# Kernel optimization log

Hardware: AMD Instinct MI355X
Metric: run time of the kernel (lower is better)

Reference implementation:

```python
import jax, jax.numpy as jnp
import numpy as np

DK_SCALE = 1.0 / np.sqrt(64.0).astype(np.float32)  # 1/sqrt(d_k)
TEMPERATURE = 1.0  # __init__ overrides temperature to 1
MASK_FILL = -1000000000.0


def setup_inputs() -> dict:
    key = jax.random.key(0)
    kq, kk, kv, km = jax.random.split(key, 4)
    B, H, S, D = 4, 16, 2048, 64
    q = jax.random.normal(kq, (B, H, S, D), dtype=jnp.float32)
    k = jax.random.normal(kk, (B, H, S, D), dtype=jnp.float32)
    v = jax.random.normal(kv, (B, H, S, D), dtype=jnp.float32)
    mask = jax.random.randint(km, (B, 1, S, S), 0, 2, dtype=jnp.int32)
    return {"q": q, "k": k, "v": v, "mask": mask}


def reference(q, k, v, mask):
    # attn = (q * scale) @ k^T  -> [B, H, S, S]
    scale = jnp.asarray(DK_SCALE / TEMPERATURE, dtype=q.dtype)
    attn = jnp.einsum("bhqd,bhkd->bhqk", q * scale, k)
    attn = jnp.where(mask == 0, jnp.asarray(MASK_FILL, dtype=attn.dtype), attn)
    attn = jax.nn.softmax(attn, axis=-1)
    out = jnp.einsum("bhqk,bhkd->bhqd", attn, v)
    return (out, attn)
```

## Files before the change

### kernel.cpp

```cpp
#include <hip/hip_runtime.h>
#include <hip/hip_bf16.h>


#define NB 4
#define NH 16
#define S_ 2048
#define D_ 64
#define QT 16
#define NW 8
#define NT 512
#define KSEG (S_ / NW)
#define SCALE 0.125f
#define MASKFILL -1000000000.0f

typedef float f32x4 __attribute__((ext_vector_type(4)));
typedef int   i32x4 __attribute__((ext_vector_type(4)));
typedef short bf16x8 __attribute__((ext_vector_type(8)));

__device__ __forceinline__ short f2bf(float x) {
  union { __hip_bfloat16 h; short s; } u;
  u.h = __float2bfloat16(x);
  return u.s;
}

__global__ __launch_bounds__(NT, 2)
void sdpa_fused(const float* __restrict__ q, const float* __restrict__ k,
                const float* __restrict__ v, const int* __restrict__ mask,
                float* __restrict__ out, float* __restrict__ attn)
{
  __shared__ float sc[QT * S_];

  const int qt   = blockIdx.x;
  const int bh   = blockIdx.y;
  const int b    = bh >> 4;
  const int tid  = threadIdx.x;
  const int wid  = tid >> 6;
  const int lane = tid & 63;
  const int l15  = lane & 15;
  const int l4   = lane >> 4;

  const float* __restrict__ qh = q + (size_t)bh * S_ * D_;
  const float* __restrict__ kh = k + (size_t)bh * S_ * D_;
  const float* __restrict__ vh = v + (size_t)bh * S_ * D_;
  const int*   __restrict__ mb = mask + (size_t)b * S_ * S_;
  const int q0 = qt * QT;

  bf16x8 aq[2];
  {
    const float* qrow = qh + (size_t)(q0 + l15) * D_ + l4 * 8;
    #pragma unroll
    for (int h = 0; h < 2; ++h) {
      f32x4 x0 = *(const f32x4*)(qrow + h * 32);
      f32x4 x1 = *(const f32x4*)(qrow + h * 32 + 4);
      bf16x8 a;
      #pragma unroll
      for (int j = 0; j < 4; ++j) {
        a[j]     = f2bf(x0[j] * SCALE);
        a[j + 4] = f2bf(x1[j] * SCALE);
      }
      aq[h] = a;
    }
  }

  const int kbase = wid * KSEG;
  #pragma unroll 2
  for (int g = 0; g < KSEG / 16; ++g) {
    const int kc = kbase + g * 16;
    const float* krow = kh + (size_t)(kc + l15) * D_ + l4 * 8;
    f32x4 acc = {0.f, 0.f, 0.f, 0.f};
    #pragma unroll
    for (int h = 0; h < 2; ++h) {
      f32x4 x0 = *(const f32x4*)(krow + h * 32);
      f32x4 x1 = *(const f32x4*)(krow + h * 32 + 4);
      bf16x8 bk;
      #pragma unroll
      for (int j = 0; j < 4; ++j) { bk[j] = f2bf(x0[j]); bk[j + 4] = f2bf(x1[j]); }
      acc = __builtin_amdgcn_mfma_f32_16x16x32_bf16(aq[h], bk, acc, 0, 0, 0);
    }
    #pragma unroll
    for (int r = 0; r < 4; ++r) {
      const int row = l4 * 4 + r;
      const int col = kc + l15;
      sc[row * S_ + ((((col >> 2) ^ row) << 2) | (col & 3))] = acc[r];
    }
  }
  __syncthreads();

  #pragma unroll
  for (int rr = 0; rr < 2; ++rr) {
    const int row = wid * 2 + rr;
    float* srow = sc + row * S_;
    const int* mrow = mb + (size_t)(q0 + row) * S_;

    f32x4 m4 = {-3.0e38f, -3.0e38f, -3.0e38f, -3.0e38f};
    for (int i = 0; i < 8; ++i) {
      const int clin = i * 64 + lane;
      const int c = (clin ^ row) << 2;
      f32x4 vv = *(f32x4*)(srow + c);
      i32x4 mm = *(const i32x4*)(mrow + clin * 4);
      #pragma unroll
      for (int j = 0; j < 4; ++j) {
        vv[j] = mm[j] ? vv[j] : MASKFILL;
        m4[j] = fmaxf(m4[j], vv[j]);
      }
      *(f32x4*)(srow + c) = vv;
    }
    float mx = fmaxf(fmaxf(m4[0], m4[1]), fmaxf(m4[2], m4[3]));
    #pragma unroll
    for (int off = 32; off >= 1; off >>= 1) mx = fmaxf(mx, __shfl_xor(mx, off));

    f32x4 s4 = {0.f, 0.f, 0.f, 0.f};
    for (int i = 0; i < 8; ++i) {
      const int c = ((i * 64 + lane) ^ row) << 2;
      f32x4 vv = *(f32x4*)(srow + c);
      f32x4 e;
      #pragma unroll
      for (int j = 0; j < 4; ++j) { e[j] = __expf(vv[j] - mx); s4[j] += e[j]; }
      *(f32x4*)(srow + c) = e;
    }
    float sm = s4[0] + s4[1] + s4[2] + s4[3];
    #pragma unroll
    for (int off = 32; off >= 1; off >>= 1) sm += __shfl_xor(sm, off);
    const float rinv = 1.0f / sm;

    float* arow = attn + ((size_t)bh * S_ + q0 + row) * S_;
    for (int i = 0; i < 8; ++i) {
      const int clin = i * 64 + lane;
      const int c = (clin ^ row) << 2;
      f32x4 vv = *(f32x4*)(srow + c);
      vv *= rinv;
      *(f32x4*)(srow + c) = vv;
      *(f32x4*)(arow + clin * 4) = vv;
    }
  }
  __syncthreads();

  f32x4 oacc[4] = {{0,0,0,0},{0,0,0,0},{0,0,0,0},{0,0,0,0}};
  #pragma unroll 2
  for (int ks = 0; ks < KSEG; ks += 32) {
    const int k0 = kbase + ks + l4 * 8;
    const float* srow = sc + l15 * S_;
    const int cc = k0 >> 2;
    f32x4 p0 = *(const f32x4*)(srow + ((cc ^ l15) << 2));
    f32x4 p1 = *(const f32x4*)(srow + (((cc + 1) ^ l15) << 2));
    bf16x8 ap;
    #pragma unroll
    for (int j = 0; j < 4; ++j) { ap[j] = f2bf(p0[j]); ap[j + 4] = f2bf(p1[j]); }
    #pragma unroll
    for (int g = 0; g < 4; ++g) {
      bf16x8 bv;
      #pragma unroll
      for (int j = 0; j < 8; ++j)
        bv[j] = f2bf(vh[(size_t)(k0 + j) * D_ + g * 16 + l15]);
      oacc[g] = __builtin_amdgcn_mfma_f32_16x16x32_bf16(ap, bv, oacc[g], 0, 0, 0);
    }
  }
  __syncthreads();

  float* part = sc;
  #pragma unroll
  for (int g = 0; g < 4; ++g) {
    #pragma unroll
    for (int r = 0; r < 4; ++r)
      part[(wid * QT + l4 * 4 + r) * D_ + g * 16 + l15] = oacc[g][r];
  }
  __syncthreads();

  float* orow = out + ((size_t)bh * S_ + q0) * D_;
  for (int o = tid; o < QT * D_; o += NT) {
    float s = 0.f;
    #pragma unroll
    for (int w = 0; w < NW; ++w) s += part[w * (QT * D_) + o];
    orow[o] = s;
  }
}

extern "C" void kernel_launch(void* const* d_in, const int* in_sizes, int n_in,
                              void* d_out, int out_size, void* d_ws, size_t ws_size,
                              hipStream_t stream) {
  const float* q    = (const float*)d_in[0];
  const float* k    = (const float*)d_in[1];
  const float* v    = (const float*)d_in[2];
  const int*   mask = (const int*)d_in[3];
  float* out  = (float*)d_out;
  float* attn = out + (size_t)NB * NH * S_ * D_;
  dim3 grid(S_ / QT, NB * NH);
  sdpa_fused<<<grid, dim3(NT), 0, stream>>>(q, k, v, mask, out, attn);
}
```

Measured before the change: 1.991 ms.

## Keep attention scores in registers and cut shared memory for higher occupancy

The 128KB shared score buffer is replaced by per-wave register accumulators (16 fragments of QK^T). Row max and sum are combined across waves through small shared buffers. Probabilities are packed as bf16 in registers, written to attn with nontemporal stores, and staged through a small per-wave LDS tile for the PV MFMA. Other changes: a 1D grid with block swizzling for L2 locality, launch bounds raised to 4 blocks per CU, and masks read directly in MFMA fragment layout. The cost is higher register pressure and normalized attn values that are rounded from bf16-packed exponentials, which lowers precision.

```diff
diff --git a/kernel.cpp b/kernel.cpp
--- a/kernel.cpp
+++ b/kernel.cpp
@@ -9,12 +9,12 @@
 #define QT 16
 #define NW 8
 #define NT 512
-#define KSEG (S_ / NW)
+#define KSEG 256
+#define NF 16
 #define SCALE 0.125f
 #define MASKFILL -1000000000.0f
 
 typedef float f32x4 __attribute__((ext_vector_type(4)));
-typedef int   i32x4 __attribute__((ext_vector_type(4)));
 typedef short bf16x8 __attribute__((ext_vector_type(8)));
 
 __device__ __forceinline__ short f2bf(float x) {
@@ -22,17 +22,33 @@
   u.h = __float2bfloat16(x);
   return u.s;
 }
-
-__global__ __launch_bounds__(NT, 2)
+__device__ __forceinline__ unsigned pack2(float a, float b) {
+  return (unsigned)(unsigned short)f2bf(a) | ((unsigned)(unsigned short)f2bf(b) << 16);
+}
+__device__ __forceinline__ float unlo(unsigned u) { return __uint_as_float(u << 16); }
+__device__ __forceinline__ float unhi(unsigned u) { return __uint_as_float(u & 0xffff0000u); }
+
+__device__ __forceinline__ void lds_fence() {
+  __builtin_amdgcn_sched_barrier(0);
+  asm volatile("s_waitcnt lgkmcnt(0)" ::: "memory");
+  __builtin_amdgcn_sched_barrier(0);
+}
+
+__global__ __launch_bounds__(NT, 4)
 void sdpa_fused(const float* __restrict__ q, const float* __restrict__ k,
                 const float* __restrict__ v, const int* __restrict__ mask,
                 float* __restrict__ out, float* __restrict__ attn)
 {
-  __shared__ float sc[QT * S_];
-
-  const int qt   = blockIdx.x;
-  const int bh   = blockIdx.y;
-  const int b    = bh >> 4;
+  __shared__ float tb[NW][2][QT][32];
+  __shared__ float mbuf[NW][QT];
+  __shared__ float lbuf[NW][QT];
+
+  const int bid = blockIdx.x;
+  const int swz = (bid & 7) * 1024 + (bid >> 3);
+  const int qt  = swz & 127;
+  const int bh  = swz >> 7;
+  const int b   = bh >> 4;
+
   const int tid  = threadIdx.x;
   const int wid  = tid >> 6;
   const int lane = tid & 63;
@@ -43,7 +59,8 @@
   const float* __restrict__ kh = k + (size_t)bh * S_ * D_;
   const float* __restrict__ vh = v + (size_t)bh * S_ * D_;
   const int*   __restrict__ mb = mask + (size_t)b * S_ * S_;
-  const int q0 = qt * QT;
+  const int q0    = qt * QT;
+  const int kbase = wid * KSEG;
 
   bf16x8 aq[2];
   {
@@ -62,116 +79,171 @@
     }
   }
 
-  const int kbase = wid * KSEG;
-  #pragma unroll 2
-  for (int g = 0; g < KSEG / 16; ++g) {
-    const int kc = kbase + g * 16;
-    const float* krow = kh + (size_t)(kc + l15) * D_ + l4 * 8;
-    f32x4 acc = {0.f, 0.f, 0.f, 0.f};
-    #pragma unroll
-    for (int h = 0; h < 2; ++h) {
-      f32x4 x0 = *(const f32x4*)(krow + h * 32);
-      f32x4 x1 = *(const f32x4*)(krow + h * 32 + 4);
-      bf16x8 bk;
-      #pragma unroll
-      for (int j = 0; j < 4; ++j) { bk[j] = f2bf(x0[j]); bk[j + 4] = f2bf(x1[j]); }
-      acc = __builtin_amdgcn_mfma_f32_16x16x32_bf16(aq[h], bk, acc, 0, 0, 0);
-    }
-    #pragma unroll
-    for (int r = 0; r < 4; ++r) {
-      const int row = l4 * 4 + r;
-      const int col = kc + l15;
-      sc[row * S_ + ((((col >> 2) ^ row) << 2) | (col & 3))] = acc[r];
-    }
+  f32x4 acc[NF];
+  {
+    const float* krow = kh + (size_t)(kbase + l15) * D_ + l4 * 8;
+    #pragma unroll
+    for (int f = 0; f < NF; ++f) {
+      f32x4 a0 = {0.f, 0.f, 0.f, 0.f};
+      #pragma unroll
+      for (int h = 0; h < 2; ++h) {
+        f32x4 x0 = *(const f32x4*)(krow + h * 32);
+        f32x4 x1 = *(const f32x4*)(krow + h * 32 + 4);
+        bf16x8 bk;
+        #pragma unroll
+        for (int j = 0; j < 4; ++j) { bk[j] = f2bf(x0[j]); bk[j + 4] = f2bf(x1[j]); }
+        a0 = __builtin_amdgcn_mfma_f32_16x16x32_bf16(aq[h], bk, a0, 0, 0, 0);
+      }
+      acc[f] = a0;
+      krow += 16 * D_;
+    }
+  }
+
+  const int* mr0 = mb + (size_t)(q0 + l4 * 4 + 0) * S_ + kbase + l15;
+  const int* mr1 = mr0 + S_;
+  const int* mr2 = mr1 + S_;
+  const int* mr3 = mr2 + S_;
+  float rmax[4] = {-3.0e38f, -3.0e38f, -3.0e38f, -3.0e38f};
+  #pragma unroll
+  for (int f = 0; f < NF; ++f) {
+    const int o = f * 16;
+    float s0 = mr0[o] ? acc[f][0] : MASKFILL;
+    float s1 = mr1[o] ? acc[f][1] : MASKFILL;
+    float s2 = mr2[o] ? acc[f][2] : MASKFILL;
+    float s3 = mr3[o] ? acc[f][3] : MASKFILL;
+    acc[f][0] = s0; acc[f][1] = s1; acc[f][2] = s2; acc[f][3] = s3;
+    rmax[0] = fmaxf(rmax[0], s0); rmax[1] = fmaxf(rmax[1], s1);
+    rmax[2] = fmaxf(rmax[2], s2); rmax[3] = fmaxf(rmax[3], s3);
+  }
+  #pragma unroll
+  for (int off = 1; off < 16; off <<= 1) {
+    #pragma unroll
+    for (int r = 0; r < 4; ++r) rmax[r] = fmaxf(rmax[r], __shfl_xor(rmax[r], off));
+  }
+  {
+    float wv = (l15 == 0) ? rmax[0] : (l15 == 1) ? rmax[1] : (l15 == 2) ? rmax[2] : rmax[3];
+    if (l15 < 4) mbuf[wid][l4 * 4 + l15] = wv;
   }
   __syncthreads();
-
-  #pragma unroll
-  for (int rr = 0; rr < 2; ++rr) {
-    const int row = wid * 2 + rr;
-    float* srow = sc + row * S_;
-    const int* mrow = mb + (size_t)(q0 + row) * S_;
-
-    f32x4 m4 = {-3.0e38f, -3.0e38f, -3.0e38f, -3.0e38f};
-    for (int i = 0; i < 8; ++i) {
-      const int clin = i * 64 + lane;
-      const int c = (clin ^ row) << 2;
-      f32x4 vv = *(f32x4*)(srow + c);
-      i32x4 mm = *(const i32x4*)(mrow + clin * 4);
-      #pragma unroll
-      for (int j = 0; j < 4; ++j) {
-        vv[j] = mm[j] ? vv[j] : MASKFILL;
-        m4[j] = fmaxf(m4[j], vv[j]);
+  float M[4];
+  {
+    f32x4 mv = *(const f32x4*)&mbuf[0][l4 * 4];
+    #pragma unroll
+    for (int w = 1; w < NW; ++w) {
+      f32x4 t = *(const f32x4*)&mbuf[w][l4 * 4];
+      #pragma unroll
+      for (int r = 0; r < 4; ++r) mv[r] = fmaxf(mv[r], t[r]);
+    }
+    #pragma unroll
+    for (int r = 0; r < 4; ++r) M[r] = mv[r];
+  }
+
+  float rsum[4] = {0.f, 0.f, 0.f, 0.f};
+  uint2 pk[NF];
+  #pragma unroll
+  for (int f = 0; f < NF; ++f) {
+    float e0 = __expf(acc[f][0] - M[0]);
+    float e1 = __expf(acc[f][1] - M[1]);
+    float e2 = __expf(acc[f][2] - M[2]);
+    float e3 = __expf(acc[f][3] - M[3]);
+    rsum[0] += e0; rsum[1] += e1; rsum[2] += e2; rsum[3] += e3;
+    pk[f].x = pack2(e0, e1);
+    pk[f].y = pack2(e2, e3);
+  }
+  #pragma unroll
+  for (int off = 1; off < 16; off <<= 1) {
+    #pragma unroll
+    for (int r = 0; r < 4; ++r) rsum[r] += __shfl_xor(rsum[r], off);
+  }
+  {
+    float wv = (l15 == 0) ? rsum[0] : (l15 == 1) ? rsum[1] : (l15 == 2) ? rsum[2] : rsum[3];
+    if (l15 < 4) lbuf[wid][l4 * 4 + l15] = wv;
+  }
+  __syncthreads();
+  float rinv[4];
+  {
+    f32x4 lv = *(const f32x4*)&lbuf[0][l4 * 4];
+    #pragma unroll
+    for (int w = 1; w < NW; ++w) {
+      f32x4 t = *(const f32x4*)&lbuf[w][l4 * 4];
+      #pragma unroll
+      for (int r = 0; r < 4; ++r) lv[r] += t[r];
+    }
+    #pragma unroll
+    for (int r = 0; r < 4; ++r) rinv[r] = 1.0f / lv[r];
+  }
+
+  {
+    float* ar0 = attn + ((size_t)bh * S_ + q0 + l4 * 4) * S_ + kbase + l15;
+    float* ar1 = ar0 + S_;
+    float* ar2 = ar1 + S_;
+    float* ar3 = ar2 + S_;
+    #pragma unroll
+    for (int f = 0; f < NF; ++f) {
+      const int o = f * 16;
+      __builtin_nontemporal_store(unlo(pk[f].x) * rinv[0], ar0 + o);
+      __builtin_nontemporal_store(unhi(pk[f].x) * rinv[1], ar1 + o);
+      __builtin_nontemporal_store(unlo(pk[f].y) * rinv[2], ar2 + o);
+      __builtin_nontemporal_store(unhi(pk[f].y) * rinv[3], ar3 + o);
+    }
+  }
+
+  f32x4 oacc[4] = {{0,0,0,0},{0,0,0,0},{0,0,0,0},{0,0,0,0}};
+  const float* vb = vh + (size_t)kbase * D_ + l15;
+  #pragma unroll
+  for (int c = 0; c < 8; ++c) {
+    const int pc = c & 1;
+    #pragma unroll
+    for (int fr = 0; fr < 2; ++fr) {
+      const int f = 2 * c + fr;
+      #pragma unroll
+      for (int r = 0; r < 4; ++r) {
+        const int row = l4 * 4 + r;
+        const int col = fr * 16 + l15;
+        const float pv_ =
+            ((r == 0) ? unlo(pk[f].x) : (r == 1) ? unhi(pk[f].x)
+             : (r == 2) ? unlo(pk[f].y) : unhi(pk[f].y)) * rinv[r];
+        tb[wid][pc][row][col ^ ((row & 7) << 2)] = pv_;
       }
-      *(f32x4*)(srow + c) = vv;
-    }
-    float mx = fmaxf(fmaxf(m4[0], m4[1]), fmaxf(m4[2], m4[3]));
-    #pragma unroll
-    for (int off = 32; off >= 1; off >>= 1) mx = fmaxf(mx, __shfl_xor(mx, off));
-
-    f32x4 s4 = {0.f, 0.f, 0.f, 0.f};
-    for (int i = 0; i < 8; ++i) {
-      const int c = ((i * 64 + lane) ^ row) << 2;
-      f32x4 vv = *(f32x4*)(srow + c);
-      f32x4 e;
-      #pragma unroll
-      for (int j = 0; j < 4; ++j) { e[j] = __expf(vv[j] - mx); s4[j] += e[j]; }
-      *(f32x4*)(srow + c) = e;
-    }
-    float sm = s4[0] + s4[1] + s4[2] + s4[3];
-    #pragma unroll
-    for (int off = 32; off >= 1; off >>= 1) sm += __shfl_xor(sm, off);
-    const float rinv = 1.0f / sm;
-
-    float* arow = attn + ((size_t)bh * S_ + q0 + row) * S_;
-    for (int i = 0; i < 8; ++i) {
-      const int clin = i * 64 + lane;
-      const int c = (clin ^ row) << 2;
-      f32x4 vv = *(f32x4*)(srow + c);
-      vv *= rinv;
-      *(f32x4*)(srow + c) = vv;
-      *(f32x4*)(arow + clin * 4) = vv;
-    }
-  }
-  __syncthreads();
-
-  f32x4 oacc[4] = {{0,0,0,0},{0,0,0,0},{0,0,0,0},{0,0,0,0}};
-  #pragma unroll 2
-  for (int ks = 0; ks < KSEG; ks += 32) {
-    const int k0 = kbase + ks + l4 * 8;
-    const float* srow = sc + l15 * S_;
-    const int cc = k0 >> 2;
-    f32x4 p0 = *(const f32x4*)(srow + ((cc ^ l15) << 2));
-    f32x4 p1 = *(const f32x4*)(srow + (((cc + 1) ^ l15) << 2));
+    }
+    lds_fence();
+    const int swzr = (l15 & 7) << 2;
+    const float* tbp = &tb[wid][pc][l15][0];
+    f32x4 p0 = *(const f32x4*)(tbp + ((l4 * 8)     ^ swzr));
+    f32x4 p1 = *(const f32x4*)(tbp + ((l4 * 8 + 4) ^ swzr));
     bf16x8 ap;
     #pragma unroll
     for (int j = 0; j < 4; ++j) { ap[j] = f2bf(p0[j]); ap[j + 4] = f2bf(p1[j]); }
+    const float* vc = vb + (size_t)(c * 32 + l4 * 8) * D_;
     #pragma unroll
     for (int g = 0; g < 4; ++g) {
       bf16x8 bv;
       #pragma unroll
-      for (int j = 0; j < 8; ++j)
-        bv[j] = f2bf(vh[(size_t)(k0 + j) * D_ + g * 16 + l15]);
+      for (int j = 0; j < 8; ++j) bv[j] = f2bf(vc[j * D_ + g * 16]);
       oacc[g] = __builtin_amdgcn_mfma_f32_16x16x32_bf16(ap, bv, oacc[g], 0, 0, 0);
     }
   }
+
+  lds_fence();
+  {
+    float* pw = &tb[0][0][0][0] + wid * (QT * D_);
+    #pragma unroll
+    for (int g = 0; g < 4; ++g) {
+      #pragma unroll
+      for (int r = 0; r < 4; ++r)
+        pw[(l4 * 4 + r) * D_ + g * 16 + l15] = oacc[g][r];
+    }
+  }
   __syncthreads();
-
-  float* part = sc;
-  #pragma unroll
-  for (int g = 0; g < 4; ++g) {
-    #pragma unroll
-    for (int r = 0; r < 4; ++r)
-      part[(wid * QT + l4 * 4 + r) * D_ + g * 16 + l15] = oacc[g][r];
-  }
-  __syncthreads();
-
-  float* orow = out + ((size_t)bh * S_ + q0) * D_;
-  for (int o = tid; o < QT * D_; o += NT) {
-    float s = 0.f;
-    #pragma unroll
-    for (int w = 0; w < NW; ++w) s += part[w * (QT * D_) + o];
-    orow[o] = s;
+  {
+    const float* pr = &tb[0][0][0][0];
+    float* orow = out + ((size_t)bh * S_ + q0) * D_;
+    for (int o = tid; o < QT * D_; o += NT) {
+      float s = 0.f;
+      #pragma unroll
+      for (int w = 0; w < NW; ++w) s += pr[w * (QT * D_) + o];
+      __builtin_nontemporal_store(s, orow + o);
+    }
   }
 }
 
@@ -184,6 +256,5 @@
   const int*   mask = (const int*)d_in[3];
   float* out  = (float*)d_out;
   float* attn = out + (size_t)NB * NH * S_ * D_;
-  dim3 grid(S_ / QT, NB * NH);
-  sdpa_fused<<<grid, dim3(NT), 0, stream>>>(q, k, v, mask, out, attn);
-}
+  sdpa_fused<<<dim3(S_ / QT * NB * NH), dim3(NT), 0, stream>>>(q, k, v, mask, out, attn);
+}
```

Result: faster. 1.734 ms (-12.9%).
